# Performance work log

Measured on AMD Instinct MI355X. Metric: run time of the kernel, lower is better.

## Reference

```python
import jax, jax.numpy as jnp
import numpy as np

B, N, D, H = 2, 2048, 768, 12
HD = D // H  # 64


def apply_rotary_embed(x, thetas):
    # x: (..., N, HD), thetas: (N, HD) broadcast over leading dims
    x1, x2 = jnp.split(x, 2, axis=-1)
    x_rot = jnp.concatenate([-x2, x1], axis=-1)
    return x * jnp.cos(thetas) + x_rot * jnp.sin(thetas)


def setup_inputs() -> dict:
    key = jax.random.key(0)
    ks = jax.random.split(key, 5)
    s = 0.02
    return {
        "x": jax.random.normal(ks[0], (B, N, D), dtype=jnp.float32),
        "pos_embed": jax.random.normal(ks[1], (N, HD), dtype=jnp.float32),
        "Wqkv": jax.random.normal(ks[2], (3 * D, D), dtype=jnp.float32) * s,
        "Wproj": jax.random.normal(ks[3], (D, D), dtype=jnp.float32) * s,
        "bproj": jnp.zeros((D,), dtype=jnp.float32),
    }


def reference(x, pos_embed, Wqkv, Wproj, bproj):
    Bb, Nn, Dd = x.shape
    # fused QKV projection (torch Linear: x @ W.T), no bias
    qkv = jnp.einsum('bnd,ed->bne', x, Wqkv)                 # (B, N, 3D)
    qkv = qkv.reshape(Bb, Nn, 3, H, HD).transpose(2, 0, 3, 1, 4)  # (3, B, H, N, HD)
    q, k, v = qkv[0], qkv[1], qkv[2]
    # rotary embedding on q and k
    q = apply_rotary_embed(q, pos_embed)
    k = apply_rotary_embed(k, pos_embed)
    # scaled dot-product attention (non-causal, no mask, no dropout)
    scale = 1.0 / jnp.sqrt(jnp.asarray(HD, dtype=x.dtype))
    scores = jnp.einsum('bhqd,bhkd->bhqk', q, k) * scale     # (B, H, N, N)
    attn = jax.nn.softmax(scores, axis=-1)
    out = jnp.einsum('bhqk,bhkd->bhqd', attn, v)             # (B, H, N, HD)
    out = out.transpose(0, 2, 1, 3).reshape(Bb, Nn, Dd)      # (B, N, D)
    # output projection (with bias)
    return jnp.einsum('bnd,ed->bne', out, Wproj) + bproj
```

## Files before the change

### kernel.cpp

```cpp
#include <hip/hip_runtime.h>
#include <stdint.h>

typedef __attribute__((ext_vector_type(8))) short short8;
typedef __attribute__((ext_vector_type(4))) float floatx4;
typedef __attribute__((ext_vector_type(16))) float floatx16;
typedef __attribute__((ext_vector_type(4))) unsigned int uintx4;

#define BB 2
#define NN 2048
#define DD 768
#define HH 12
#define HDD 64
#define MM (BB*NN)

__device__ __forceinline__ unsigned short f2bf(float f) {
  unsigned int u = __builtin_bit_cast(unsigned int, f);
  u += 0x7fffu + ((u >> 16) & 1u);
  return (unsigned short)(u >> 16);
}
__device__ __forceinline__ float bf2f(unsigned short u) {
  unsigned int v = ((unsigned int)u) << 16;
  return __builtin_bit_cast(float, v);
}

__device__ __forceinline__ void gld16(const unsigned short* g, unsigned short* l) {
  __builtin_amdgcn_global_load_lds(
      (const __attribute__((address_space(1))) void*)g,
      (__attribute__((address_space(3))) void*)l, 16, 0, 0);
}

__device__ __forceinline__ unsigned int cvtpk_bf16(float a, float b) {
  unsigned int r;
  asm("v_cvt_pk_bf16_f32 %0, %1, %2" : "=v"(r) : "v"(a), "v"(b));
  return r;
}
__device__ __forceinline__ void plswap(unsigned int& a, unsigned int& b) {
  asm("v_permlane32_swap_b32 %0, %1" : "+v"(a), "+v"(b));
}

__global__ void cvt_all(const float* __restrict__ x, const float* __restrict__ wq,
                        const float* __restrict__ wp, unsigned short* __restrict__ xb,
                        unsigned short* __restrict__ wqb, unsigned short* __restrict__ wpb) {
  const int n1 = MM*DD/4, n2 = 3*DD*DD/4, n3 = DD*DD/4;
  int i = blockIdx.x * blockDim.x + threadIdx.x;
  const float* s; unsigned short* d; int j;
  if (i < n1)            { s = x;  d = xb;  j = i; }
  else if (i < n1+n2)    { s = wq; d = wqb; j = i - n1; }
  else if (i < n1+n2+n3) { s = wp; d = wpb; j = i - n1 - n2; }
  else return;
  float4 v = reinterpret_cast<const float4*>(s)[j];
  unsigned int lo = (unsigned int)f2bf(v.x) | ((unsigned int)f2bf(v.y) << 16);
  unsigned int hi = (unsigned int)f2bf(v.z) | ((unsigned int)f2bf(v.w) << 16);
  reinterpret_cast<uint2*>(d)[j] = make_uint2(lo, hi);
}

template<int MODE, int MT, int NT, int BK>
__global__ __launch_bounds__(256) void gemm_bt(
    const unsigned short* __restrict__ A,
    const unsigned short* __restrict__ Bt,
    void* __restrict__ Cout, const float* __restrict__ bias,
    int Nn, int K,
    const float* __restrict__ pos,
    unsigned short* __restrict__ qb2, unsigned short* __restrict__ kb2,
    unsigned short* __restrict__ vb2)
{
  constexpr int MTC = MT / 32;
  constexpr int NTC = NT / 32;
  constexpr int PARTS = BK / 8;
  __shared__ __align__(16) unsigned short as_[MT*BK];
  __shared__ __align__(16) unsigned short bs_[NT*BK];
  const int t = threadIdx.x;
  const int w = t >> 6, lane = t & 63;
  const int quad = lane >> 4, l16 = lane & 15;
  const int wm = (w >> 1) * (MT/2), wn = (w & 1) * (NT/2);
  const int m0 = blockIdx.y * MT, n0 = blockIdx.x * NT;

  const floatx4 fz = {0.f, 0.f, 0.f, 0.f};
  floatx4 acc[MTC][NTC];
#pragma unroll
  for (int mt = 0; mt < MTC; mt++)
#pragma unroll
    for (int nt = 0; nt < NTC; nt++) acc[mt][nt] = fz;

  for (int k0 = 0; k0 < K; k0 += BK) {
    __syncthreads();
#pragma unroll
    for (int i = 0; i < MT*PARTS/256; i++) {
      int c = t + i * 256;
      int row = c / PARTS, part = c % PARTS;
      int sp = part ^ (row & (PARTS-1));
      gld16(&A[(size_t)(m0 + row)*K + k0 + sp*8], &as_[c*8]);
    }
#pragma unroll
    for (int i = 0; i < NT*PARTS/256; i++) {
      int c = t + i * 256;
      int row = c / PARTS, part = c % PARTS;
      int sp = part ^ (row & (PARTS-1));
      gld16(&Bt[(size_t)(n0 + row)*K + k0 + sp*8], &bs_[c*8]);
    }
    __syncthreads();
#pragma unroll
    for (int kh = 0; kh < BK/32; kh++) {
      short8 af[MTC], bfr[NTC];
#pragma unroll
      for (int mt = 0; mt < MTC; mt++) {
        int row = wm + mt*16 + l16;
        int slot = (kh*4 + quad) ^ (row & (PARTS-1));
        af[mt] = *reinterpret_cast<const short8*>(&as_[row*BK + slot*8]);
      }
#pragma unroll
      for (int nt = 0; nt < NTC; nt++) {
        int row = wn + nt*16 + l16;
        int slot = (kh*4 + quad) ^ (row & (PARTS-1));
        bfr[nt] = *reinterpret_cast<const short8*>(&bs_[row*BK + slot*8]);
      }
#pragma unroll
      for (int mt = 0; mt < MTC; mt++)
#pragma unroll
        for (int nt = 0; nt < NTC; nt++)
          acc[mt][nt] = __builtin_amdgcn_mfma_f32_16x16x32_bf16(af[mt], bfr[nt], acc[mt][nt], 0, 0, 0);
    }
  }
  if (MODE == 2) {
    const int region = n0 / DD;
    const int nl0 = n0 - region * DD;
    const int head = (nl0 + wn) / HDD;
    if (region < 2) {
#pragma unroll
      for (int mt = 0; mt < MTC; mt++)
#pragma unroll
        for (int r = 0; r < 4; r++) {
          int gm = m0 + wm + mt*16 + quad*4 + r;
          int bq = gm >> 11, nseq = gm & (NN-1);
          size_t base = ((size_t)(bq*HH + head)*NN + nseq) * HDD;
#pragma unroll
          for (int nt = 0; nt < 2; nt++) {
            int hd = nt*16 + l16;
            float t1 = pos[nseq*HDD + hd], t2 = pos[nseq*HDD + hd + 32];
            float s1, c1, s2, c2;
            __sincosf(t1, &s1, &c1);
            __sincosf(t2, &s2, &c2);
            float a1 = acc[mt][nt][r], a2 = acc[mt][nt+2][r];
            if (region == 0) {
              qb2[base + hd]      = f2bf((a1*c1 - a2*s1) * 0.125f);
              qb2[base + hd + 32] = f2bf((a2*c2 + a1*s2) * 0.125f);
            } else {
              int sl1 = (hd >> 3) ^ (nseq & 7);
              int sl2 = ((hd >> 3) + 4) ^ (nseq & 7);
              kb2[base + sl1*8 + (hd & 7)] = f2bf(a1*c1 - a2*s1);
              kb2[base + sl2*8 + (hd & 7)] = f2bf(a2*c2 + a1*s2);
            }
          }
        }
    } else {
#pragma unroll
      for (int mt = 0; mt < MTC; mt++)
#pragma unroll
        for (int nt = 0; nt < NTC; nt++) {
          int hd = nt*16 + l16;
          int seqb = m0 + wm + mt*16 + quad*4;
          int bq = seqb >> 11, nsb = seqb & (NN-1);
          unsigned int p0 = (unsigned int)f2bf(acc[mt][nt][0]) | ((unsigned int)f2bf(acc[mt][nt][1]) << 16);
          unsigned int p1 = (unsigned int)f2bf(acc[mt][nt][2]) | ((unsigned int)f2bf(acc[mt][nt][3]) << 16);
          int slot = ((nsb >> 3) & 15) ^ (hd & 7);
          size_t addr = ((size_t)(bq*HH + head)*HDD + hd) * NN + (nsb & ~127) + slot*8 + (nsb & 7);
          *(uint2*)&vb2[addr] = make_uint2(p0, p1);
        }
    }
  } else {
#pragma unroll
    for (int mt = 0; mt < MTC; mt++)
#pragma unroll
      for (int nt = 0; nt < NTC; nt++)
#pragma unroll
        for (int r = 0; r < 4; r++) {
          int gm = m0 + wm + mt*16 + quad*4 + r;
          int gn = n0 + wn + nt*16 + l16;
          float v = acc[mt][nt][r];
          if (MODE == 0)
            reinterpret_cast<unsigned short*>(Cout)[(size_t)gm * Nn + gn] = f2bf(v);
          else
            reinterpret_cast<float*>(Cout)[(size_t)gm * Nn + gn] = v + bias[gn];
        }
  }
}

__global__ __launch_bounds__(256, 4) void flash_attn(
    const unsigned short* __restrict__ qb, const unsigned short* __restrict__ kb,
    const unsigned short* __restrict__ vb, unsigned short* __restrict__ ob)
{
  __shared__ __align__(16) unsigned short ks[128*64];
  __shared__ __align__(16) unsigned short vt[64*128];
  __shared__ __align__(16) float lsd[128];
  const int qt = blockIdx.x, bh = blockIdx.y;
  const int b = bh / HH, hh = bh % HH;
  const int t = threadIdx.x;
  const int w = t >> 6, lane = t & 63;
  const int l32 = lane & 31, hf = lane >> 5;
  const int gq = w >> 1;
  const int kh = w & 1;
  const int q0 = qt * 64;
  const size_t kbase = (size_t)bh * (NN*HDD);

  short8 qf[4];
  {
    const unsigned short* qp = &qb[((size_t)bh*NN + q0 + gq*32 + l32)*HDD + hf*8];
#pragma unroll
    for (int s = 0; s < 4; s++) qf[s] = *(const short8*)&qp[s*16];
  }
  floatx16 fz16;
#pragma unroll
  for (int z = 0; z < 16; z++) fz16[z] = 0.f;
  floatx16 oacc[2];
  oacc[0] = fz16; oacc[1] = fz16;
  float lrow = 0.f;

  for (int kt = 0; kt < NN/128; kt++) {
    __syncthreads();
#pragma unroll
    for (int i = 0; i < 4; i++) {
      int c = i*256 + t;
      gld16(&kb[kbase + (size_t)kt*8192 + c*8], &ks[c*8]);
      gld16(&vb[kbase + (size_t)(c >> 4)*NN + kt*128 + (c & 15)*8], &vt[c*8]);
    }
    __syncthreads();

    short8 pfr[4];
    float rs = 0.f;
#pragma unroll
    for (int tt = 0; tt < 2; tt++) {
      int t2 = kh*2 + tt;
      int row = t2*32 + l32;
      floatx16 acc;
#pragma unroll
      for (int z = 0; z < 16; z++) acc[z] = 0.f;
      __builtin_amdgcn_s_setprio(1);
#pragma unroll
      for (int s = 0; s < 4; s++) {
        int cd = (2*s + hf) ^ (l32 & 7);
        short8 kf = *(const short8*)&ks[row*64 + cd*8];
        acc = __builtin_amdgcn_mfma_f32_32x32x16_bf16(kf, qf[s], acc, 0, 0, 0);
      }
      __builtin_amdgcn_s_setprio(0);
      float pv_[16];
#pragma unroll
      for (int r = 0; r < 16; r++) { pv_[r] = __expf(acc[r]); rs += pv_[r]; }
      unsigned int w0 = cvtpk_bf16(pv_[0],  pv_[1]);
      unsigned int w1 = cvtpk_bf16(pv_[2],  pv_[3]);
      unsigned int w2 = cvtpk_bf16(pv_[4],  pv_[5]);
      unsigned int w3 = cvtpk_bf16(pv_[6],  pv_[7]);
      unsigned int w4 = cvtpk_bf16(pv_[8],  pv_[9]);
      unsigned int w5 = cvtpk_bf16(pv_[10], pv_[11]);
      unsigned int w6 = cvtpk_bf16(pv_[12], pv_[13]);
      unsigned int w7 = cvtpk_bf16(pv_[14], pv_[15]);
      plswap(w0, w2); plswap(w1, w3);
      plswap(w4, w6); plswap(w5, w7);
      uintx4 ua = {w0, w1, w2, w3};
      uintx4 ub = {w4, w5, w6, w7};
      pfr[2*tt+0] = __builtin_bit_cast(short8, ua);
      pfr[2*tt+1] = __builtin_bit_cast(short8, ub);
    }
    rs += __shfl_xor(rs, 32);
    lrow += rs;
    __builtin_amdgcn_s_setprio(1);
#pragma unroll
    for (int ss = 0; ss < 4; ss++) {
      int s2 = kh*4 + ss;
      int ca = (s2*2 + hf) ^ (l32 & 7);
      short8 pf = pfr[ss];
#pragma unroll
      for (int ht = 0; ht < 2; ht++) {
        int hd = ht*32 + l32;
        short8 vf = *(const short8*)&vt[hd*128 + ca*8];
        oacc[ht] = __builtin_amdgcn_mfma_f32_32x32x16_bf16(pf, vf, oacc[ht], 0, 0, 0);
      }
    }
    __builtin_amdgcn_s_setprio(0);
  }
  __syncthreads();
  float* om = (float*)ks;
  if (kh) {
    float* base = om + gq*2048;
#pragma unroll
    for (int ht = 0; ht < 2; ht++)
#pragma unroll
      for (int g = 0; g < 4; g++)
#pragma unroll
        for (int e = 0; e < 4; e++) {
          int ql = hf*4 + g*8 + e;
          base[ql*64 + ht*32 + l32] = oacc[ht][4*g+e];
        }
  }
  if (hf == 0) lsd[w*32 + l32] = lrow;
  __syncthreads();
  if (!kh) {
    float* base = om + gq*2048;
#pragma unroll
    for (int g = 0; g < 4; g++)
#pragma unroll
      for (int e = 0; e < 4; e++) {
        int ql = hf*4 + g*8 + e;
        float l = lsd[gq*64 + ql] + lsd[gq*64 + 32 + ql];
        float inv = 1.f / l;
        int qrow = q0 + gq*32 + ql;
#pragma unroll
        for (int ht = 0; ht < 2; ht++) {
          float v = oacc[ht][4*g+e] + base[ql*64 + ht*32 + l32];
          ob[((size_t)(b*NN + qrow))*DD + hh*HDD + ht*32 + l32] = f2bf(v * inv);
        }
      }
  }
}

extern "C" void kernel_launch(void* const* d_in, const int* in_sizes, int n_in,
                              void* d_out, int out_size, void* d_ws, size_t ws_size,
                              hipStream_t stream)
{
  const float* x     = (const float*)d_in[0];
  const float* pos   = (const float*)d_in[1];
  const float* Wqkv  = (const float*)d_in[2];
  const float* Wproj = (const float*)d_in[3];
  const float* bproj = (const float*)d_in[4];

  unsigned short* p = (unsigned short*)d_ws;
  unsigned short* xb     = p; p += (size_t)MM*DD;
  unsigned short* wqkvb  = p; p += (size_t)3*DD*DD;
  unsigned short* wprojb = p; p += (size_t)DD*DD;
  unsigned short* ob     = p; p += (size_t)MM*DD;
  unsigned short* qb     = p; p += (size_t)BB*HH*NN*HDD;
  unsigned short* kb     = p; p += (size_t)BB*HH*NN*HDD;
  unsigned short* vb     = p; p += (size_t)BB*HH*NN*HDD;

  const int ncvt = MM*DD/4 + 3*DD*DD/4 + DD*DD/4;
  cvt_all<<<ncvt/256, 256, 0, stream>>>(x, Wqkv, Wproj, xb, wqkvb, wprojb);

  gemm_bt<2,64,128,64><<<dim3(3*DD/128, MM/64), 256, 0, stream>>>(
      xb, wqkvb, nullptr, nullptr, 3*DD, DD, pos, qb, kb, vb);
  flash_attn<<<dim3(NN/64, BB*HH), 256, 0, stream>>>(qb, kb, vb, ob);
  gemm_bt<1,64,64,64><<<dim3(DD/64, MM/64), 256, 0, stream>>>(
      ob, wprojb, (float*)d_out, bproj, DD, DD, nullptr, nullptr, nullptr, nullptr);
}
```

Before: 155.6 us.

## Split flash attention key tiles across four waves per query group with 512 threads

Doubles the flash attention block to 512 threads (8 waves), so each wave handles one 32-key slice of every 128-key tile instead of two. Per-wave work and register pressure drop, which allows a higher occupancy target. The partial outputs from the four key-split waves are then combined through shared memory in a two-stage tree reduction with an extra barrier. The costs are more cross-wave reduction traffic, more synchronization, and each wave re-issuing its share of the Q fragments.

```diff
diff --git a/kernel.cpp b/kernel.cpp
--- a/kernel.cpp
+++ b/kernel.cpp
@@ -185,20 +185,21 @@
   }
 }
 
-__global__ __launch_bounds__(256, 4) void flash_attn(
+__global__ __launch_bounds__(512, 6) void flash_attn(
     const unsigned short* __restrict__ qb, const unsigned short* __restrict__ kb,
     const unsigned short* __restrict__ vb, unsigned short* __restrict__ ob)
 {
-  __shared__ __align__(16) unsigned short ks[128*64];
-  __shared__ __align__(16) unsigned short vt[64*128];
-  __shared__ __align__(16) float lsd[128];
+  __shared__ __align__(16) unsigned short smem[128*64 + 64*128];
+  __shared__ float lsd[256];
+  unsigned short* ks = smem;
+  unsigned short* vt = smem + 128*64;
   const int qt = blockIdx.x, bh = blockIdx.y;
   const int b = bh / HH, hh = bh % HH;
   const int t = threadIdx.x;
   const int w = t >> 6, lane = t & 63;
   const int l32 = lane & 31, hf = lane >> 5;
-  const int gq = w >> 1;
-  const int kh = w & 1;
+  const int gq = w >> 2;
+  const int kh = w & 3;
   const int q0 = qt * 64;
   const size_t kbase = (size_t)bh * (NN*HDD);
 
@@ -218,56 +219,51 @@
   for (int kt = 0; kt < NN/128; kt++) {
     __syncthreads();
 #pragma unroll
-    for (int i = 0; i < 4; i++) {
-      int c = i*256 + t;
+    for (int i = 0; i < 2; i++) {
+      int c = i*512 + t;
       gld16(&kb[kbase + (size_t)kt*8192 + c*8], &ks[c*8]);
       gld16(&vb[kbase + (size_t)(c >> 4)*NN + kt*128 + (c & 15)*8], &vt[c*8]);
     }
     __syncthreads();
 
-    short8 pfr[4];
+    const int row = kh*32 + l32;
+    floatx16 acc;
+#pragma unroll
+    for (int z = 0; z < 16; z++) acc[z] = 0.f;
+    __builtin_amdgcn_s_setprio(1);
+#pragma unroll
+    for (int s = 0; s < 4; s++) {
+      int cd = (2*s + hf) ^ (l32 & 7);
+      short8 kf = *(const short8*)&ks[row*64 + cd*8];
+      acc = __builtin_amdgcn_mfma_f32_32x32x16_bf16(kf, qf[s], acc, 0, 0, 0);
+    }
+    __builtin_amdgcn_s_setprio(0);
+    float pv_[16];
     float rs = 0.f;
 #pragma unroll
-    for (int tt = 0; tt < 2; tt++) {
-      int t2 = kh*2 + tt;
-      int row = t2*32 + l32;
-      floatx16 acc;
-#pragma unroll
-      for (int z = 0; z < 16; z++) acc[z] = 0.f;
-      __builtin_amdgcn_s_setprio(1);
-#pragma unroll
-      for (int s = 0; s < 4; s++) {
-        int cd = (2*s + hf) ^ (l32 & 7);
-        short8 kf = *(const short8*)&ks[row*64 + cd*8];
-        acc = __builtin_amdgcn_mfma_f32_32x32x16_bf16(kf, qf[s], acc, 0, 0, 0);
-      }
-      __builtin_amdgcn_s_setprio(0);
-      float pv_[16];
-#pragma unroll
-      for (int r = 0; r < 16; r++) { pv_[r] = __expf(acc[r]); rs += pv_[r]; }
-      unsigned int w0 = cvtpk_bf16(pv_[0],  pv_[1]);
-      unsigned int w1 = cvtpk_bf16(pv_[2],  pv_[3]);
-      unsigned int w2 = cvtpk_bf16(pv_[4],  pv_[5]);
-      unsigned int w3 = cvtpk_bf16(pv_[6],  pv_[7]);
-      unsigned int w4 = cvtpk_bf16(pv_[8],  pv_[9]);
-      unsigned int w5 = cvtpk_bf16(pv_[10], pv_[11]);
-      unsigned int w6 = cvtpk_bf16(pv_[12], pv_[13]);
-      unsigned int w7 = cvtpk_bf16(pv_[14], pv_[15]);
-      plswap(w0, w2); plswap(w1, w3);
-      plswap(w4, w6); plswap(w5, w7);
-      uintx4 ua = {w0, w1, w2, w3};
-      uintx4 ub = {w4, w5, w6, w7};
-      pfr[2*tt+0] = __builtin_bit_cast(short8, ua);
-      pfr[2*tt+1] = __builtin_bit_cast(short8, ub);
-    }
+    for (int r = 0; r < 16; r++) { pv_[r] = __expf(acc[r]); rs += pv_[r]; }
+    unsigned int w0 = cvtpk_bf16(pv_[0],  pv_[1]);
+    unsigned int w1 = cvtpk_bf16(pv_[2],  pv_[3]);
+    unsigned int w2 = cvtpk_bf16(pv_[4],  pv_[5]);
+    unsigned int w3 = cvtpk_bf16(pv_[6],  pv_[7]);
+    unsigned int w4 = cvtpk_bf16(pv_[8],  pv_[9]);
+    unsigned int w5 = cvtpk_bf16(pv_[10], pv_[11]);
+    unsigned int w6 = cvtpk_bf16(pv_[12], pv_[13]);
+    unsigned int w7 = cvtpk_bf16(pv_[14], pv_[15]);
+    plswap(w0, w2); plswap(w1, w3);
+    plswap(w4, w6); plswap(w5, w7);
+    uintx4 ua = {w0, w1, w2, w3};
+    uintx4 ub = {w4, w5, w6, w7};
+    short8 pfr0 = __builtin_bit_cast(short8, ua);
+    short8 pfr1 = __builtin_bit_cast(short8, ub);
     rs += __shfl_xor(rs, 32);
     lrow += rs;
     __builtin_amdgcn_s_setprio(1);
 #pragma unroll
-    for (int ss = 0; ss < 4; ss++) {
-      int s2 = kh*4 + ss;
+    for (int ss = 0; ss < 2; ss++) {
+      int s2 = kh*2 + ss;
       int ca = (s2*2 + hf) ^ (l32 & 7);
-      short8 pf = pfr[ss];
+      short8 pf = ss ? pfr1 : pfr0;
 #pragma unroll
       for (int ht = 0; ht < 2; ht++) {
         int hd = ht*32 + l32;
@@ -278,9 +274,9 @@
     __builtin_amdgcn_s_setprio(0);
   }
   __syncthreads();
-  float* om = (float*)ks;
-  if (kh) {
-    float* base = om + gq*2048;
+  float* om = (float*)smem;
+  if (kh & 1) {
+    float* base = om + (gq*2 + (kh>>1))*2048;
 #pragma unroll
     for (int ht = 0; ht < 2; ht++)
 #pragma unroll
@@ -293,14 +289,39 @@
   }
   if (hf == 0) lsd[w*32 + l32] = lrow;
   __syncthreads();
-  if (!kh) {
-    float* base = om + gq*2048;
+  if (!(kh & 1)) {
+    float* base = om + (gq*2 + (kh>>1))*2048;
+#pragma unroll
+    for (int ht = 0; ht < 2; ht++)
+#pragma unroll
+      for (int g = 0; g < 4; g++)
+#pragma unroll
+        for (int e = 0; e < 4; e++) {
+          int ql = hf*4 + g*8 + e;
+          oacc[ht][4*g+e] += base[ql*64 + ht*32 + l32];
+        }
+    if (kh == 2) {
+#pragma unroll
+      for (int ht = 0; ht < 2; ht++)
+#pragma unroll
+        for (int g = 0; g < 4; g++)
+#pragma unroll
+          for (int e = 0; e < 4; e++) {
+            int ql = hf*4 + g*8 + e;
+            base[ql*64 + ht*32 + l32] = oacc[ht][4*g+e];
+          }
+    }
+  }
+  __syncthreads();
+  if (kh == 0) {
+    float* base = om + (gq*2 + 1)*2048;
 #pragma unroll
     for (int g = 0; g < 4; g++)
 #pragma unroll
       for (int e = 0; e < 4; e++) {
         int ql = hf*4 + g*8 + e;
-        float l = lsd[gq*64 + ql] + lsd[gq*64 + 32 + ql];
+        float l = lsd[(gq*4 + 0)*32 + ql] + lsd[(gq*4 + 1)*32 + ql]
+                + lsd[(gq*4 + 2)*32 + ql] + lsd[(gq*4 + 3)*32 + ql];
         float inv = 1.f / l;
         int qrow = q0 + gq*32 + ql;
 #pragma unroll
@@ -336,7 +357,7 @@
 
   gemm_bt<2,64,128,64><<<dim3(3*DD/128, MM/64), 256, 0, stream>>>(
       xb, wqkvb, nullptr, nullptr, 3*DD, DD, pos, qb, kb, vb);
-  flash_attn<<<dim3(NN/64, BB*HH), 256, 0, stream>>>(qb, kb, vb, ob);
+  flash_attn<<<dim3(NN/64, BB*HH), 512, 0, stream>>>(qb, kb, vb, ob);
   gemm_bt<1,64,64,64><<<dim3(DD/64, MM/64), 256, 0, stream>>>(
       ob, wprojb, (float*)d_out, bproj, DD, DD, nullptr, nullptr, nullptr, nullptr);
 }
```

Result: slower. 203.1 us (+30.5%).

## Double-buffer K/V tiles in flash attention with 64-key stages

Applied to the files above, without the earlier changes.

Restructures the flash attention key loop from single-buffered 128-key tiles into a two-buffer ping-pong of 64-key tiles. The next tile is loaded while the current one is computed, with one barrier per stage instead of two. The aim is to hide global-to-LDS load latency behind the MFMA and exp work. In exchange each stage does less work per barrier. The V layout changes to a 64-wide row stride, and the swizzle and index math must still match how the data is stored.

```diff
diff --git a/kernel.cpp b/kernel.cpp
--- a/kernel.cpp
+++ b/kernel.cpp
@@ -189,13 +189,12 @@
     const unsigned short* __restrict__ qb, const unsigned short* __restrict__ kb,
     const unsigned short* __restrict__ vb, unsigned short* __restrict__ ob)
 {
-  __shared__ __align__(16) unsigned short ks[128*64];
-  __shared__ __align__(16) unsigned short vt[64*128];
-  __shared__ __align__(16) float lsd[128];
+  __shared__ __align__(16) unsigned short smem[2*8192];
+  __shared__ float lsd[128];
   const int qt = blockIdx.x, bh = blockIdx.y;
   const int b = bh / HH, hh = bh % HH;
-  const int t = threadIdx.x;
-  const int w = t >> 6, lane = t & 63;
+  const int tid = threadIdx.x;
+  const int w = tid >> 6, lane = tid & 63;
   const int l32 = lane & 31, hf = lane >> 5;
   const int gq = w >> 1;
   const int kh = w & 1;
@@ -215,70 +214,83 @@
   oacc[0] = fz16; oacc[1] = fz16;
   float lrow = 0.f;
 
-  for (int kt = 0; kt < NN/128; kt++) {
-    __syncthreads();
-#pragma unroll
-    for (int i = 0; i < 4; i++) {
-      int c = i*256 + t;
-      gld16(&kb[kbase + (size_t)kt*8192 + c*8], &ks[c*8]);
-      gld16(&vb[kbase + (size_t)(c >> 4)*NN + kt*128 + (c & 15)*8], &vt[c*8]);
-    }
-    __syncthreads();
-
-    short8 pfr[4];
+  auto stage = [&](int buf, int t) {
+    unsigned short* kd = smem + buf*8192;
+    unsigned short* vd = smem + buf*8192 + 4096;
+#pragma unroll
+    for (int i = 0; i < 2; i++) {
+      int c = i*256 + tid;
+      gld16(&kb[kbase + (size_t)(t*64 + (c >> 3))*64 + (c & 7)*8], &kd[c*8]);
+    }
+#pragma unroll
+    for (int i = 0; i < 2; i++) {
+      int c = i*256 + tid;
+      gld16(&vb[kbase + (size_t)(c >> 3)*NN + t*64 + (c & 7)*8], &vd[c*8]);
+    }
+  };
+
+  auto compute = [&](int buf) {
+    const unsigned short* kc = smem + buf*8192;
+    const unsigned short* vc = smem + buf*8192 + 4096;
+    const int row = kh*32 + l32;
+    floatx16 acc;
+#pragma unroll
+    for (int z = 0; z < 16; z++) acc[z] = 0.f;
+    __builtin_amdgcn_s_setprio(1);
+#pragma unroll
+    for (int s = 0; s < 4; s++) {
+      int cd = (2*s + hf) ^ (l32 & 7);
+      short8 kf = *(const short8*)&kc[row*64 + cd*8];
+      acc = __builtin_amdgcn_mfma_f32_32x32x16_bf16(kf, qf[s], acc, 0, 0, 0);
+    }
+    __builtin_amdgcn_s_setprio(0);
+    float pv_[16];
     float rs = 0.f;
 #pragma unroll
-    for (int tt = 0; tt < 2; tt++) {
-      int t2 = kh*2 + tt;
-      int row = t2*32 + l32;
-      floatx16 acc;
-#pragma unroll
-      for (int z = 0; z < 16; z++) acc[z] = 0.f;
-      __builtin_amdgcn_s_setprio(1);
-#pragma unroll
-      for (int s = 0; s < 4; s++) {
-        int cd = (2*s + hf) ^ (l32 & 7);
-        short8 kf = *(const short8*)&ks[row*64 + cd*8];
-        acc = __builtin_amdgcn_mfma_f32_32x32x16_bf16(kf, qf[s], acc, 0, 0, 0);
-      }
-      __builtin_amdgcn_s_setprio(0);
-      float pv_[16];
-#pragma unroll
-      for (int r = 0; r < 16; r++) { pv_[r] = __expf(acc[r]); rs += pv_[r]; }
-      unsigned int w0 = cvtpk_bf16(pv_[0],  pv_[1]);
-      unsigned int w1 = cvtpk_bf16(pv_[2],  pv_[3]);
-      unsigned int w2 = cvtpk_bf16(pv_[4],  pv_[5]);
-      unsigned int w3 = cvtpk_bf16(pv_[6],  pv_[7]);
-      unsigned int w4 = cvtpk_bf16(pv_[8],  pv_[9]);
-      unsigned int w5 = cvtpk_bf16(pv_[10], pv_[11]);
-      unsigned int w6 = cvtpk_bf16(pv_[12], pv_[13]);
-      unsigned int w7 = cvtpk_bf16(pv_[14], pv_[15]);
-      plswap(w0, w2); plswap(w1, w3);
-      plswap(w4, w6); plswap(w5, w7);
-      uintx4 ua = {w0, w1, w2, w3};
-      uintx4 ub = {w4, w5, w6, w7};
-      pfr[2*tt+0] = __builtin_bit_cast(short8, ua);
-      pfr[2*tt+1] = __builtin_bit_cast(short8, ub);
-    }
+    for (int r = 0; r < 16; r++) { pv_[r] = __expf(acc[r]); rs += pv_[r]; }
+    unsigned int w0 = cvtpk_bf16(pv_[0],  pv_[1]);
+    unsigned int w1 = cvtpk_bf16(pv_[2],  pv_[3]);
+    unsigned int w2 = cvtpk_bf16(pv_[4],  pv_[5]);
+    unsigned int w3 = cvtpk_bf16(pv_[6],  pv_[7]);
+    unsigned int w4 = cvtpk_bf16(pv_[8],  pv_[9]);
+    unsigned int w5 = cvtpk_bf16(pv_[10], pv_[11]);
+    unsigned int w6 = cvtpk_bf16(pv_[12], pv_[13]);
+    unsigned int w7 = cvtpk_bf16(pv_[14], pv_[15]);
+    plswap(w0, w2); plswap(w1, w3);
+    plswap(w4, w6); plswap(w5, w7);
+    uintx4 ua = {w0, w1, w2, w3};
+    uintx4 ub = {w4, w5, w6, w7};
+    short8 pfr0 = __builtin_bit_cast(short8, ua);
+    short8 pfr1 = __builtin_bit_cast(short8, ub);
     rs += __shfl_xor(rs, 32);
     lrow += rs;
     __builtin_amdgcn_s_setprio(1);
 #pragma unroll
-    for (int ss = 0; ss < 4; ss++) {
-      int s2 = kh*4 + ss;
-      int ca = (s2*2 + hf) ^ (l32 & 7);
-      short8 pf = pfr[ss];
+    for (int ss = 0; ss < 2; ss++) {
+      int ca = (kh*4 + ss*2 + hf) ^ (l32 & 7);
+      short8 pf = ss ? pfr1 : pfr0;
 #pragma unroll
       for (int ht = 0; ht < 2; ht++) {
         int hd = ht*32 + l32;
-        short8 vf = *(const short8*)&vt[hd*128 + ca*8];
+        short8 vf = *(const short8*)&vc[hd*64 + ca*8];
         oacc[ht] = __builtin_amdgcn_mfma_f32_32x32x16_bf16(pf, vf, oacc[ht], 0, 0, 0);
       }
     }
     __builtin_amdgcn_s_setprio(0);
-  }
+  };
+
+  stage(0, 0);
   __syncthreads();
-  float* om = (float*)ks;
+  for (int t = 0; t < NN/64; t += 2) {
+    if (t + 1 < NN/64) stage(1, t + 1);
+    compute(0);
+    __syncthreads();
+    if (t + 2 < NN/64) stage(0, t + 2);
+    compute(1);
+    __syncthreads();
+  }
+
+  float* om = (float*)smem;
   if (kh) {
     float* base = om + gq*2048;
 #pragma unroll
```

After: 156.1 us. No clear change (+0.3%).
